# Kernel optimization log

Measured on AMD Instinct MI355X. Metric: run time of the kernel, lower is better.

## Reference

```python
import jax, jax.numpy as jnp
import numpy as np

D_MODEL, N_HEAD, D_FF = 768, 12, 3072
HEAD_DIM = D_MODEL // N_HEAD
EPS = 1e-5


def _layernorm(x, g, b):
    mu = jnp.mean(x, axis=-1, keepdims=True)
    var = jnp.mean((x - mu) ** 2, axis=-1, keepdims=True)
    return (x - mu) * jax.lax.rsqrt(var + EPS) * g + b


def setup_inputs() -> dict:
    key = jax.random.key(0)
    ks = jax.random.split(key, 14)
    s = 1.0 / np.sqrt(D_MODEL)
    sf = 1.0 / np.sqrt(D_FF)
    inp = {
        "x": jax.random.normal(ks[0], (2, 2048, D_MODEL), dtype=jnp.float32),
        "Wq": jax.random.normal(ks[1], (D_MODEL, D_MODEL), dtype=jnp.float32) * s,
        "bq": jnp.zeros((D_MODEL,), jnp.float32),
        "Wk": jax.random.normal(ks[2], (D_MODEL, D_MODEL), dtype=jnp.float32) * s,
        "bk": jnp.zeros((D_MODEL,), jnp.float32),
        "Wv": jax.random.normal(ks[3], (D_MODEL, D_MODEL), dtype=jnp.float32) * s,
        "bv": jnp.zeros((D_MODEL,), jnp.float32),
        "Wo": jax.random.normal(ks[4], (D_MODEL, D_MODEL), dtype=jnp.float32) * s,
        "bo": jnp.zeros((D_MODEL,), jnp.float32),
        "W1": jax.random.normal(ks[5], (D_MODEL, D_FF), dtype=jnp.float32) * s,
        "b1": jnp.zeros((D_FF,), jnp.float32),
        "W2": jax.random.normal(ks[6], (D_FF, D_MODEL), dtype=jnp.float32) * sf,
        "b2": jnp.zeros((D_MODEL,), jnp.float32),
        "ln1_g": jnp.ones((D_MODEL,), jnp.float32),
        "ln1_b": jnp.zeros((D_MODEL,), jnp.float32),
        "ln2_g": jnp.ones((D_MODEL,), jnp.float32),
        "ln2_b": jnp.zeros((D_MODEL,), jnp.float32),
    }
    return inp


def reference(x, Wq, bq, Wk, bk, Wv, bv, Wo, bo, W1, b1, W2, b2,
              ln1_g, ln1_b, ln2_g, ln2_b):
    B, S, D = x.shape
    # projections -> [B, H, S, hd]
    def proj(W, b):
        return (x @ W + b).reshape(B, S, N_HEAD, HEAD_DIM).transpose(0, 2, 1, 3)
    q, k, v = proj(Wq, bq), proj(Wk, bk), proj(Wv, bv)
    scores = jnp.einsum("bhqd,bhkd->bhqk", q, k) / jnp.sqrt(
        jnp.asarray(HEAD_DIM, jnp.float32))
    attn = jax.nn.softmax(scores, axis=-1)
    ctx = jnp.einsum("bhqk,bhkd->bhqd", attn, v)
    ctx = ctx.transpose(0, 2, 1, 3).reshape(B, S, D)
    attn_out = ctx @ Wo + bo
    h = _layernorm(x + attn_out, ln1_g, ln1_b)
    ffn = jax.nn.gelu(h @ W1 + b1, approximate=False) @ W2 + b2
    return _layernorm(h + ffn, ln2_g, ln2_b)
```

## Files before the change

### kernel.cpp

```cpp
#include <hip/hip_runtime.h>
#include <hip/hip_bf16.h>
#include <cstdint>
#include <cstddef>

typedef unsigned short u16;
typedef __bf16 bf16x8 __attribute__((ext_vector_type(8)));
typedef float f32x4 __attribute__((ext_vector_type(4)));

#define MFMA_BF16(a, b, c) __builtin_amdgcn_mfma_f32_16x16x32_bf16((a), (b), (c), 0, 0, 0)

#define GLDS16(g, l)                                                        \
  __builtin_amdgcn_global_load_lds(                                         \
      (__attribute__((address_space(1))) void*)(void*)(g),                  \
      (__attribute__((address_space(3))) void*)(void*)(l), 16, 0, 0)

#define QSCALE 0.18033688011112042f
#define PSTRIDE ((size_t)4096 * 768)
#define KVSPLIT 2

__device__ __forceinline__ u16 f2bf(float x) {
  union { float f; unsigned u; } c; c.f = x;
  unsigned u = c.u;
  unsigned r = (u + 0x7fffu + ((u >> 16) & 1u)) >> 16;
  return (u16)r;
}
__device__ __forceinline__ float bf2f(u16 x) {
  union { unsigned u; float f; } c; c.u = (unsigned)x << 16; return c.f;
}

__global__ __launch_bounds__(256) void prep_weights_k(
    const float* __restrict__ Wq, const float* __restrict__ Wk,
    const float* __restrict__ Wv, const float* __restrict__ Wo,
    const float* __restrict__ W1, const float* __restrict__ W2,
    const float* __restrict__ bq, const float* __restrict__ bk,
    const float* __restrict__ bv, const float* __restrict__ x,
    u16* __restrict__ WqkvT, u16* __restrict__ WoT,
    u16* __restrict__ W1T, u16* __restrict__ W2T, float* __restrict__ bqkv,
    u16* __restrict__ xb) {
  const int id = blockIdx.x;
  if (id >= 6921) {
    const int i = ((id - 6921) * 256 + threadIdx.x) * 4;
    const float4 v = *(const float4*)(x + i);
    ushort4 o;
    o.x = f2bf(v.x); o.y = f2bf(v.y); o.z = f2bf(v.z); o.w = f2bf(v.w);
    *(ushort4*)(xb + i) = o;
    return;
  }
  if (id >= 6912) {
    int i = (id - 6912) * 256 + threadIdx.x;
    if (i < 768) bqkv[i] = bq[i];
    else if (i < 1536) bqkv[i] = bk[i - 768];
    else if (i < 2304) bqkv[i] = bv[i - 1536];
    return;
  }
  const float* in; u16* out; int K, N, bx, by;
  if (id < 2304) {
    const int mat = id / 576, t = id - mat * 576;
    in = (mat == 0) ? Wq : (mat == 1) ? Wk : (mat == 2) ? Wv : Wo;
    out = (mat == 0) ? WqkvT : (mat == 1) ? WqkvT + 768 * 768
        : (mat == 2) ? WqkvT + 2 * 768 * 768 : WoT;
    K = 768; N = 768; bx = (t % 24) * 32; by = (t / 24) * 32;
  } else if (id < 4608) {
    const int t = id - 2304;
    in = W1; out = W1T; K = 768; N = 3072;
    bx = (t % 96) * 32; by = (t / 96) * 32;
  } else {
    const int t = id - 4608;
    in = W2; out = W2T; K = 3072; N = 768;
    bx = (t % 24) * 32; by = (t / 24) * 32;
  }
  __shared__ float tile[32][33];
  const int tx = threadIdx.x & 31, ty = threadIdx.x >> 5;
#pragma unroll
  for (int j = 0; j < 32; j += 8)
    tile[ty + j][tx] = in[(size_t)(by + ty + j) * N + bx + tx];
  __syncthreads();
#pragma unroll
  for (int j = 0; j < 32; j += 8)
    out[(size_t)(bx + ty + j) * K + by + tx] = f2bf(tile[tx][ty + j]);
}

template <int EPI>
__global__ __launch_bounds__(256) void gemm_bt(
    const u16* __restrict__ A, const u16* __restrict__ BT,
    const float* __restrict__ bias, int M, int N, int K, int kchunk,
    float* __restrict__ outf, u16* __restrict__ outb,
    u16* __restrict__ qo, u16* __restrict__ ko, u16* __restrict__ vto) {
  __shared__ __align__(16) u16 lsA[2 * 128 * 32];
  __shared__ __align__(16) u16 lsB[2 * 128 * 32];
  const int tid = threadIdx.x;
  const int w = tid >> 6, lane = tid & 63;
  const int wm = w & 1, wn = w >> 1;
  const int lrow = lane & 15, quad = lane >> 4;
  const int m0 = blockIdx.y * 128, n0 = blockIdx.x * 128;
  const int kbeg = blockIdx.z * kchunk;

  f32x4 acc[4][4];
#pragma unroll
  for (int i = 0; i < 4; ++i)
#pragma unroll
    for (int j = 0; j < 4; ++j) acc[i][j] = (f32x4){0.f, 0.f, 0.f, 0.f};

  const int off = tid * 16;
  const int line = tid >> 3;
  const int slotp = tid & 7;
  const int p = slotp ^ (line & 7);
  const int srow = line * 2 + (p >> 2);
  const int scol = (p & 3) * 8;

  const u16* ga0 = A + (size_t)(m0 + srow) * K + scol;
  const u16* gb0 = BT + (size_t)(n0 + srow) * K + scol;

  auto stage = [&](int k0, int buf) {
    char* da = (char*)(lsA + buf * 4096);
    char* db = (char*)(lsB + buf * 4096);
    GLDS16(ga0 + k0, da + off);
    GLDS16(ga0 + k0 + (size_t)64 * K, da + 4096 + off);
    GLDS16(gb0 + k0, db + off);
    GLDS16(gb0 + k0 + (size_t)64 * K, db + 4096 + off);
  };

  const int lline = lrow >> 1;
  const int lslot = (((lrow & 1) << 2) + quad) ^ ((lrow >> 1) & 7);
  const int rdoff = lslot * 8;

  const int niter = kchunk >> 5;
  stage(kbeg, 0);
  for (int t = 0; t < niter; ++t) {
    __syncthreads();
    if (t + 1 < niter) stage(kbeg + (t + 1) * 32, (t + 1) & 1);
    const u16* Ab = lsA + (t & 1) * 4096;
    const u16* Bb = lsB + (t & 1) * 4096;
    bf16x8 af[4], bfr[4];
#pragma unroll
    for (int ms = 0; ms < 4; ++ms)
      af[ms] = *(const bf16x8*)&Ab[(wm * 32 + ms * 8 + lline) * 64 + rdoff];
#pragma unroll
    for (int ns = 0; ns < 4; ++ns)
      bfr[ns] = *(const bf16x8*)&Bb[(wn * 32 + ns * 8 + lline) * 64 + rdoff];
#pragma unroll
    for (int ms = 0; ms < 4; ++ms)
#pragma unroll
      for (int ns = 0; ns < 4; ++ns)
        acc[ms][ns] = MFMA_BF16(af[ms], bfr[ns], acc[ms][ns]);
  }

  u16* const pb = (EPI == 3) ? outb + (size_t)blockIdx.z * PSTRIDE : outb;
#pragma unroll
  for (int ms = 0; ms < 4; ++ms) {
    const int rbase = m0 + wm * 64 + ms * 16 + quad * 4;
#pragma unroll
    for (int ns = 0; ns < 4; ++ns) {
      const int col = n0 + wn * 64 + ns * 16 + lrow;
      if constexpr (EPI == 3) {
#pragma unroll
        for (int r = 0; r < 4; ++r)
          pb[(size_t)(rbase + r) * N + col] = f2bf(acc[ms][ns][r]);
      } else if constexpr (EPI == 2) {
        const float bcol = bias[col];
#pragma unroll
        for (int r = 0; r < 4; ++r) {
          float v = acc[ms][ns][r] + bcol;
          float g = 0.5f * v * (1.0f + erff(v * 0.7071067811865476f));
          outb[(size_t)(rbase + r) * N + col] = f2bf(g);
        }
      } else {
        const float bcol = bias[col];
        const int which = col / 768;
        const int rem = col - which * 768;
        const int hh = rem >> 6, dd = rem & 63;
        const int bI = rbase >> 11, sI = rbase & 2047;
        const size_t bh = (size_t)bI * 12 + hh;
        if (which == 0) {
#pragma unroll
          for (int r = 0; r < 4; ++r)
            qo[(bh * 2048 + sI + r) * 64 + dd] = f2bf((acc[ms][ns][r] + bcol) * QSCALE);
        } else if (which == 1) {
#pragma unroll
          for (int r = 0; r < 4; ++r)
            ko[(bh * 2048 + sI + r) * 64 + dd] = f2bf(acc[ms][ns][r] + bcol);
        } else {
          ushort4 pk;
          pk.x = f2bf(acc[ms][ns][0] + bcol);
          pk.y = f2bf(acc[ms][ns][1] + bcol);
          pk.z = f2bf(acc[ms][ns][2] + bcol);
          pk.w = f2bf(acc[ms][ns][3] + bcol);
          *(ushort4*)(vto + (bh * 64 + dd) * 2048 + sI) = pk;
        }
      }
    }
  }
}

__global__ __launch_bounds__(256) void attn_kernel(
    const u16* __restrict__ q, const u16* __restrict__ k,
    const u16* __restrict__ vT, u16* __restrict__ opart,
    float* __restrict__ lpart) {
  __shared__ __align__(16) u16 lsK[2 * 64 * 64];
  __shared__ __align__(16) u16 lsV[2 * 64 * 64];
  __shared__ __align__(16) u16 lsP[4][32 * 64];
  const int tid = threadIdx.x;
  const int w = tid >> 6, lane = tid & 63;
  const int lrow = lane & 15, quad = lane >> 4;
  const int bhz = blockIdx.x;
  const int bh = bhz % 24, z = bhz / 24;
  const int b = bh / 12, h = bh - b * 12;
  const int q0 = blockIdx.y * 128;
  const int kvbeg = z * (2048 / KVSPLIT);

  const u16* qbase = q + (size_t)bh * 2048 * 64;
  const u16* kbase = k + (size_t)bh * 2048 * 64;
  const u16* vbase = vT + (size_t)bh * 64 * 2048;

  bf16x8 qf[2][2];
#pragma unroll
  for (int m = 0; m < 2; ++m) {
    const int qrow = q0 + w * 32 + m * 16 + lrow;
    qf[m][0] = *(const bf16x8*)(qbase + (size_t)qrow * 64 + quad * 8);
    qf[m][1] = *(const bf16x8*)(qbase + (size_t)qrow * 64 + 32 + quad * 8);
  }

  float lsum[2][4] = {{0.f, 0.f, 0.f, 0.f}, {0.f, 0.f, 0.f, 0.f}};
  f32x4 oacc[2][4];
#pragma unroll
  for (int m = 0; m < 2; ++m)
#pragma unroll
    for (int d = 0; d < 4; ++d) oacc[m][d] = (f32x4){0.f, 0.f, 0.f, 0.f};

  const int off = tid * 16;
  const int srow = off >> 7;
  const int schunk = (off >> 4) & 7;
  const int sxc = schunk ^ (srow & 7);
  const int ksrc = srow * 64 + sxc * 8;
  const int vsrc0 = srow * 2048 + sxc * 8;

  const int c0 = quad ^ (lrow & 7);
  const int rd0 = c0 * 8, rd1 = (c0 ^ 4) * 8;

  u16* const lsPw = &lsP[w][0];
  const int jhi_base = lrow >> 3, jlo = lrow & 7;

  auto stage = [&](int kt, int buf) {
    char* dk = (char*)(lsK + buf * 4096);
    char* dv = (char*)(lsV + buf * 4096);
    GLDS16(kbase + (size_t)kt * 64 + ksrc, dk + off);
    GLDS16(kbase + (size_t)(kt + 32) * 64 + ksrc, dk + 4096 + off);
    GLDS16(vbase + vsrc0 + kt, dv + off);
    GLDS16(vbase + vsrc0 + kt + 32 * 2048, dv + 4096 + off);
  };

  const int ntiles = 2048 / KVSPLIT / 64;
  stage(kvbeg, 0);
  for (int t = 0; t < ntiles; ++t) {
    __syncthreads();
    if (t + 1 < ntiles) stage(kvbeg + (t + 1) * 64, (t + 1) & 1);
    const u16* Kb = lsK + (t & 1) * 4096;
    const u16* Vb = lsV + (t & 1) * 4096;

    f32x4 sc[2][4];
#pragma unroll
    for (int ns = 0; ns < 4; ++ns) {
      const u16* kr = Kb + (ns * 16 + lrow) * 64;
      bf16x8 kf0 = *(const bf16x8*)(kr + rd0);
      bf16x8 kf1 = *(const bf16x8*)(kr + rd1);
#pragma unroll
      for (int m = 0; m < 2; ++m) {
        sc[m][ns] = (f32x4){0.f, 0.f, 0.f, 0.f};
        sc[m][ns] = MFMA_BF16(qf[m][0], kf0, sc[m][ns]);
        sc[m][ns] = MFMA_BF16(qf[m][1], kf1, sc[m][ns]);
      }
    }

#pragma unroll
    for (int m = 0; m < 2; ++m)
#pragma unroll
      for (int ns = 0; ns < 4; ++ns) {
        const int jhi = ns * 2 + jhi_base;
#pragma unroll
        for (int r = 0; r < 4; ++r) {
          float p = __builtin_amdgcn_exp2f(sc[m][ns][r]);
          lsum[m][r] += p;
          union { float f; unsigned u; } cv; cv.f = p;
          const int row7 = (quad * 4 + r) & 7;
          lsPw[(m * 16 + quad * 4 + r) * 64 + ((jhi ^ row7) * 8) + jlo] =
              (u16)(cv.u >> 16);
        }
      }

#pragma unroll
    for (int d = 0; d < 4; ++d) {
      const u16* vr = Vb + (d * 16 + lrow) * 64;
      bf16x8 vf0 = *(const bf16x8*)(vr + rd0);
      bf16x8 vf1 = *(const bf16x8*)(vr + rd1);
#pragma unroll
      for (int m = 0; m < 2; ++m) {
        const u16* pr = lsPw + (m * 16 + lrow) * 64;
        bf16x8 pf0 = *(const bf16x8*)(pr + rd0);
        bf16x8 pf1 = *(const bf16x8*)(pr + rd1);
        oacc[m][d] = MFMA_BF16(pf0, vf0, oacc[m][d]);
        oacc[m][d] = MFMA_BF16(pf1, vf1, oacc[m][d]);
      }
    }
  }

#pragma unroll
  for (int m = 0; m < 2; ++m)
#pragma unroll
    for (int r = 0; r < 4; ++r) {
#pragma unroll
      for (int mm = 1; mm <= 8; mm <<= 1)
        lsum[m][r] += __shfl_xor(lsum[m][r], mm);
    }

  u16* const op = opart + (size_t)z * PSTRIDE;
#pragma unroll
  for (int m = 0; m < 2; ++m) {
    const int srow_out = q0 + w * 32 + m * 16 + quad * 4;
#pragma unroll
    for (int d = 0; d < 4; ++d)
#pragma unroll
      for (int r = 0; r < 4; ++r)
        op[(size_t)(b * 2048 + srow_out + r) * 768 + h * 64 + d * 16 + lrow] =
            f2bf(oacc[m][d][r]);
    if (lrow == 0) {
#pragma unroll
      for (int r = 0; r < 4; ++r)
        lpart[(size_t)(z * 24 + bh) * 2048 + srow_out + r] = lsum[m][r];
    }
  }
}

__global__ __launch_bounds__(256) void attn_combine_k(
    const u16* __restrict__ op, const float* __restrict__ lp,
    u16* __restrict__ ctx) {
  const unsigned idx = (blockIdx.x * 256u + threadIdx.x) * 4u;
  const unsigned row = idx / 768u;
  const unsigned c = idx - row * 768u;
  const int b = row >> 11, s = row & 2047;
  const int h = c >> 6;
  const size_t li = (size_t)(b * 12 + h) * 2048 + s;
  float l = 0.f;
  float sx = 0.f, sy = 0.f, sz = 0.f, sw = 0.f;
#pragma unroll
  for (int p = 0; p < KVSPLIT; ++p) {
    l += lp[(size_t)p * 24 * 2048 + li];
    ushort4 o = *(const ushort4*)(op + (size_t)p * PSTRIDE + idx);
    sx += bf2f(o.x); sy += bf2f(o.y); sz += bf2f(o.z); sw += bf2f(o.w);
  }
  const float rinv = 1.f / l;
  ushort4 out;
  out.x = f2bf(sx * rinv); out.y = f2bf(sy * rinv);
  out.z = f2bf(sz * rinv); out.w = f2bf(sw * rinv);
  *(ushort4*)(ctx + idx) = out;
}

__global__ __launch_bounds__(256) void ln_kernel(
    const u16* __restrict__ parts, int nparts, const float* __restrict__ bias,
    const float* __restrict__ res, const float* __restrict__ g,
    const float* __restrict__ bb, float* __restrict__ outf, u16* __restrict__ outb) {
  const int row = blockIdx.x;
  const int tid = threadIdx.x;
  const float* pr = res + (size_t)row * 768;
  float v[3], s = 0.f, s2 = 0.f;
#pragma unroll
  for (int j = 0; j < 3; ++j) {
    const int c = tid + j * 256;
    float t = bias[c] + pr[c];
    for (int p = 0; p < nparts; ++p)
      t += bf2f(parts[p * PSTRIDE + (size_t)row * 768 + c]);
    v[j] = t; s += t; s2 += t * t;
  }
#pragma unroll
  for (int m = 32; m > 0; m >>= 1) {
    s += __shfl_xor(s, m);
    s2 += __shfl_xor(s2, m);
  }
  __shared__ float red[8];
  const int w = tid >> 6, lane = tid & 63;
  if (lane == 0) { red[w] = s; red[4 + w] = s2; }
  __syncthreads();
  s = red[0] + red[1] + red[2] + red[3];
  s2 = red[4] + red[5] + red[6] + red[7];
  const float mu = s * (1.f / 768.f);
  const float var = s2 * (1.f / 768.f) - mu * mu;
  const float rstd = rsqrtf(var + 1e-5f);
#pragma unroll
  for (int j = 0; j < 3; ++j) {
    const int c = tid + j * 256;
    const float y = (v[j] - mu) * rstd * g[c] + bb[c];
    if (outf) outf[(size_t)row * 768 + c] = y;
    if (outb) outb[(size_t)row * 768 + c] = f2bf(y);
  }
}

extern "C" void kernel_launch(void* const* d_in, const int* in_sizes, int n_in,
                              void* d_out, int out_size, void* d_ws, size_t ws_size,
                              hipStream_t stream) {
  const float* x    = (const float*)d_in[0];
  const float* Wq   = (const float*)d_in[1];
  const float* bq   = (const float*)d_in[2];
  const float* Wk   = (const float*)d_in[3];
  const float* bk   = (const float*)d_in[4];
  const float* Wv   = (const float*)d_in[5];
  const float* bv   = (const float*)d_in[6];
  const float* Wo   = (const float*)d_in[7];
  const float* bo   = (const float*)d_in[8];
  const float* W1   = (const float*)d_in[9];
  const float* b1   = (const float*)d_in[10];
  const float* W2   = (const float*)d_in[11];
  const float* b2   = (const float*)d_in[12];
  const float* ln1g = (const float*)d_in[13];
  const float* ln1b = (const float*)d_in[14];
  const float* ln2g = (const float*)d_in[15];
  const float* ln2b = (const float*)d_in[16];

  char* ws = (char*)d_ws;
  size_t off = 0;
  auto alloc = [&](size_t bytes) {
    void* p = ws + off;
    off += (bytes + 255) & ~(size_t)255;
    return p;
  };
  u16*  WqkvT = (u16*)alloc(2304ull * 768 * 2);
  u16*  WoT   = (u16*)alloc(768ull * 768 * 2);
  u16*  W1T   = (u16*)alloc(3072ull * 768 * 2);
  u16*  W2T   = (u16*)alloc(768ull * 3072 * 2);
  float* bqkv = (float*)alloc(2304 * 4);
  char* bigbase = (char*)alloc(0);
  u16*  xb    = (u16*)alloc(4096ull * 768 * 2);
  u16*  qb    = (u16*)alloc(24ull * 2048 * 64 * 2);
  u16*  kb    = (u16*)alloc(24ull * 2048 * 64 * 2);
  u16*  vtb   = (u16*)alloc(24ull * 64 * 2048 * 2);
  u16*  ctx   = (u16*)alloc(4096ull * 768 * 2);
  float* lpart = (float*)alloc((size_t)KVSPLIT * 24 * 2048 * 4);
  float* hbuf  = (float*)alloc(4096ull * 768 * 4);
  u16*  hb    = (u16*)alloc(4096ull * 768 * 2);
  u16*  f1    = (u16*)alloc(4096ull * 3072 * 2);
  u16*  wop   = (u16*)bigbase;
  u16*  f2bp  = (u16*)bigbase;
  u16*  opart = (u16*)hbuf;

  prep_weights_k<<<9993, 256, 0, stream>>>(Wq, Wk, Wv, Wo, W1, W2, bq, bk, bv, x,
                                           WqkvT, WoT, W1T, W2T, bqkv, xb);

  gemm_bt<0><<<dim3(18, 32, 1), 256, 0, stream>>>(xb, WqkvT, bqkv, 4096, 2304, 768, 768,
                                                  nullptr, nullptr, qb, kb, vtb);
  attn_kernel<<<dim3(24 * KVSPLIT, 16, 1), 256, 0, stream>>>(qb, kb, vtb, opart, lpart);
  attn_combine_k<<<3072, 256, 0, stream>>>(opart, lpart, ctx);
  gemm_bt<3><<<dim3(6, 32, 2), 256, 0, stream>>>(ctx, WoT, nullptr, 4096, 768, 768, 384,
                                                 nullptr, wop, nullptr, nullptr, nullptr);
  ln_kernel<<<4096, 256, 0, stream>>>(wop, 2, bo, x, ln1g, ln1b, hbuf, hb);
  gemm_bt<2><<<dim3(24, 32, 1), 256, 0, stream>>>(hb, W1T, b1, 4096, 3072, 768, 768,
                                                  nullptr, f1, nullptr, nullptr, nullptr);
  gemm_bt<3><<<dim3(6, 32, 4), 256, 0, stream>>>(f1, W2T, nullptr, 4096, 768, 3072, 768,
                                                 nullptr, f2bp, nullptr, nullptr, nullptr);
  ln_kernel<<<4096, 256, 0, stream>>>(f2bp, 4, b2, hbuf, ln2g, ln2b, (float*)d_out, nullptr);
}
```

Before: 297.1 us.

## Load K and V fragments directly from global memory instead of LDS staging

The attention kernel stops double-buffering K and V tiles into shared memory with async global-to-LDS copies. Each lane now reads its MFMA operand fragments straight from global memory (relying on L1/L2), which drops the per-tile __syncthreads and the LDS footprint for K/V. This cuts barrier overhead and may raise occupancy, but each wave now fetches K/V separately, so global and cache traffic grow and latency is no longer hidden by prefetching.

Result: slower. 349.3 us (+17.6%).

```diff
diff --git a/kernel.cpp b/kernel.cpp
--- a/kernel.cpp
+++ b/kernel.cpp
@@ -196,8 +196,6 @@
     const u16* __restrict__ q, const u16* __restrict__ k,
     const u16* __restrict__ vT, u16* __restrict__ opart,
     float* __restrict__ lpart) {
-  __shared__ __align__(16) u16 lsK[2 * 64 * 64];
-  __shared__ __align__(16) u16 lsV[2 * 64 * 64];
   __shared__ __align__(16) u16 lsP[4][32 * 64];
   const int tid = threadIdx.x;
   const int w = tid >> 6, lane = tid & 63;
@@ -227,42 +225,25 @@
 #pragma unroll
     for (int d = 0; d < 4; ++d) oacc[m][d] = (f32x4){0.f, 0.f, 0.f, 0.f};
 
-  const int off = tid * 16;
-  const int srow = off >> 7;
-  const int schunk = (off >> 4) & 7;
-  const int sxc = schunk ^ (srow & 7);
-  const int ksrc = srow * 64 + sxc * 8;
-  const int vsrc0 = srow * 2048 + sxc * 8;
-
   const int c0 = quad ^ (lrow & 7);
   const int rd0 = c0 * 8, rd1 = (c0 ^ 4) * 8;
 
   u16* const lsPw = &lsP[w][0];
   const int jhi_base = lrow >> 3, jlo = lrow & 7;
 
-  auto stage = [&](int kt, int buf) {
-    char* dk = (char*)(lsK + buf * 4096);
-    char* dv = (char*)(lsV + buf * 4096);
-    GLDS16(kbase + (size_t)kt * 64 + ksrc, dk + off);
-    GLDS16(kbase + (size_t)(kt + 32) * 64 + ksrc, dk + 4096 + off);
-    GLDS16(vbase + vsrc0 + kt, dv + off);
-    GLDS16(vbase + vsrc0 + kt + 32 * 2048, dv + 4096 + off);
-  };
+  const u16* krow = kbase + (size_t)lrow * 64 + quad * 8;
+  const u16* vrow = vbase + (size_t)lrow * 2048 + quad * 8;
 
   const int ntiles = 2048 / KVSPLIT / 64;
-  stage(kvbeg, 0);
   for (int t = 0; t < ntiles; ++t) {
-    __syncthreads();
-    if (t + 1 < ntiles) stage(kvbeg + (t + 1) * 64, (t + 1) & 1);
-    const u16* Kb = lsK + (t & 1) * 4096;
-    const u16* Vb = lsV + (t & 1) * 4096;
+    const int kt = kvbeg + t * 64;
 
     f32x4 sc[2][4];
 #pragma unroll
     for (int ns = 0; ns < 4; ++ns) {
-      const u16* kr = Kb + (ns * 16 + lrow) * 64;
-      bf16x8 kf0 = *(const bf16x8*)(kr + rd0);
-      bf16x8 kf1 = *(const bf16x8*)(kr + rd1);
+      const u16* kr = krow + (size_t)(kt + ns * 16) * 64;
+      bf16x8 kf0 = *(const bf16x8*)(kr);
+      bf16x8 kf1 = *(const bf16x8*)(kr + 32);
 #pragma unroll
       for (int m = 0; m < 2; ++m) {
         sc[m][ns] = (f32x4){0.f, 0.f, 0.f, 0.f};
@@ -289,9 +270,9 @@
 
 #pragma unroll
     for (int d = 0; d < 4; ++d) {
-      const u16* vr = Vb + (d * 16 + lrow) * 64;
-      bf16x8 vf0 = *(const bf16x8*)(vr + rd0);
-      bf16x8 vf1 = *(const bf16x8*)(vr + rd1);
+      const u16* vr = vrow + (size_t)(d * 16) * 2048 + kt;
+      bf16x8 vf0 = *(const bf16x8*)(vr);
+      bf16x8 vf1 = *(const bf16x8*)(vr + 32);
 #pragma unroll
       for (int m = 0; m < 2; ++m) {
         const u16* pr = lsPw + (m * 16 + lrow) * 64;
```
